# Optimization experiments

Measured on AMD Instinct MI355X. Metric: run time of the kernel, lower is better.

The kernel has to match this reference:

```python
import jax, jax.numpy as jnp
import numpy as np
from jax import lax
from functools import partial

NPOINT = 2048
RADIUS = 1.0
NSAMPLE = 32


def _fps(xyz, npoint):
    # Farthest point sampling, sequential as in the classic CUDA kernel.
    # xyz: (N, 3) -> (npoint,) int32 indices; starts at index 0.
    N = xyz.shape[0]
    init_d = jnp.full((N,), jnp.inf, dtype=xyz.dtype)

    def step(carry, _):
        dists, last = carry
        delta = xyz - xyz[last]                      # (N, 3)
        nd = jnp.sum(delta * delta, axis=-1)         # (N,)
        dists = jnp.minimum(dists, nd)
        nxt = jnp.argmax(dists).astype(jnp.int32)
        return (dists, nxt), last

    (_, _), idxs = lax.scan(step, (init_d, jnp.int32(0)), None, length=npoint)
    return idxs


def _ball_query(radius, nsample, xyz, new_xyz):
    # xyz: (N, 3), new_xyz: (S, 3) -> (S, nsample) int32.
    # Take the first nsample points (in original order) within radius of each
    # centroid; pad with the first found index (centroid itself always hits).
    N = xyz.shape[0]
    d2 = (jnp.sum(new_xyz * new_xyz, -1, keepdims=True)
          + jnp.sum(xyz * xyz, -1)[None, :]
          - 2.0 * new_xyz @ xyz.T)                   # (S, N)
    mask = d2 < radius * radius
    key = jnp.where(mask, jnp.arange(N, dtype=jnp.int32), jnp.int32(N))  # (S, N)
    neg_topk, _ = lax.top_k(-key, nsample)           # nsample smallest keys
    idx = -neg_topk                                  # (S, nsample), ascending
    first = idx[:, :1]
    return jnp.where(idx == N, first, idx)


def setup_inputs() -> dict:
    key = jax.random.key(0)
    inputs = jax.random.normal(key, (4, 8192, 16), dtype=jnp.float32)
    return {"inputs": inputs}


def reference(inputs):
    xyz = inputs[..., :3]                            # (B, N, 3)
    points = inputs[..., 3:]                         # (B, N, C)

    fps_idx = jax.vmap(lambda p: _fps(p, NPOINT))(xyz)          # (B, S)
    new_xyz = jnp.take_along_axis(xyz, fps_idx[..., None], axis=1)  # (B, S, 3)

    idx = jax.vmap(partial(_ball_query, RADIUS, NSAMPLE))(xyz, new_xyz)  # (B, S, K)

    gather = jax.vmap(lambda p, i: p[i])             # (N, C), (S, K) -> (S, K, C)
    grouped_xyz = gather(xyz, idx) - new_xyz[:, :, None, :]      # (B, S, K, 3)
    grouped_points = gather(points, idx)                         # (B, S, K, C)
    new_points = jnp.concatenate([grouped_xyz, grouped_points], axis=-1)
    return new_xyz, new_points, idx, grouped_xyz
```

## Files before the change

### kernel.cpp

```cpp
#include <hip/hip_runtime.h>

#pragma clang fp contract(off)

#define NPOINT 2048
#define NSAMPLE 32
#define NPTS 8192
#define NB 4
#define CH 16
#define FPS_THREADS 512
#define PTS_PER_THREAD (NPTS / FPS_THREADS)
#define PAIRS (PTS_PER_THREAD / 2)

typedef unsigned long long u64;
typedef float v2f __attribute__((ext_vector_type(2)));

#define OFF_NEWXYZ 0
#define OFF_NEWPTS (NB * NPOINT * 3)
#define OFF_IDX (OFF_NEWPTS + NB * NPOINT * NSAMPLE * CH)
#define OFF_GXYZ (OFF_IDX + NB * NPOINT * NSAMPLE)

template <int CTRL>
__device__ __forceinline__ float dpp_fmax(float v) {
  int o = __builtin_amdgcn_update_dpp(0, __float_as_int(v), CTRL, 0xf, 0xf, true);
  return fmaxf(v, __int_as_float(o));
}

__global__ __launch_bounds__(FPS_THREADS)
__attribute__((amdgpu_waves_per_eu(2))) void fps_kernel(
    const float* __restrict__ in, float* __restrict__ out) {
  __shared__ float4 lpxyz[NPTS];
  __shared__ float newb[NPOINT * 3];
  __shared__ u64 kslot[3];

  const int b = blockIdx.x;
  const int tid = threadIdx.x;
  const float* base = in + (size_t)b * NPTS * CH;

  v2f pxv[PAIRS], pyv[PAIRS], pzv[PAIRS], dv[PAIRS];
#pragma unroll
  for (int jp = 0; jp < PAIRS; ++jp) {
    int p0 = tid * PTS_PER_THREAD + 2 * jp;
    float4 r0 = *reinterpret_cast<const float4*>(base + (size_t)p0 * CH);
    float4 r1 = *reinterpret_cast<const float4*>(base + (size_t)(p0 + 1) * CH);
    pxv[jp] = (v2f){r0.x, r1.x};
    pyv[jp] = (v2f){r0.y, r1.y};
    pzv[jp] = (v2f){r0.z, r1.z};
    lpxyz[p0] = r0;
    lpxyz[p0 + 1] = r1;
    dv[jp] = (v2f){__builtin_inff(), __builtin_inff()};
  }
  if (tid == 0) {
    kslot[0] = ((u64)0x7f800000u << 32) | 8191u;
    kslot[1] = 0;
    kslot[2] = 0;
  }

  int rd = 0, at = 1, rs = 2;
  for (int it = 0; it < NPOINT; ++it) {
    __syncthreads();
    const u64 k = kslot[rd];
    const int gi = 8191 - (int)(unsigned)k;
    const float4 g = lpxyz[gi];
    const float gx = g.x, gy = g.y, gz = g.z;
    if (tid == 0) {
      kslot[rs] = 0;
      newb[it * 3 + 0] = gx;
      newb[it * 3 + 1] = gy;
      newb[it * 3 + 2] = gz;
    }
    float bestv = -1.0f;
#pragma unroll
    for (int jp = 0; jp < PAIRS; ++jp) {
      v2f dx = pxv[jp] - gx;
      v2f dy = pyv[jp] - gy;
      v2f dz = pzv[jp] - gz;
      v2f nd = (dx * dx + dy * dy) + dz * dz;
      v2f dn = {fminf(dv[jp].x, nd.x), fminf(dv[jp].y, nd.y)};
      dv[jp] = dn;
      bestv = fmaxf(fmaxf(bestv, dn.x), dn.y);
    }
    const float* df = (const float*)dv;
    int bestj = 0;
#pragma unroll
    for (int jj = PTS_PER_THREAD - 1; jj >= 0; --jj)
      if (df[jj] == bestv) bestj = jj;
    const int besti = tid * PTS_PER_THREAD + bestj;
    float wm = bestv;
    wm = dpp_fmax<0x111>(wm);
    wm = dpp_fmax<0x112>(wm);
    wm = dpp_fmax<0x114>(wm);
    wm = dpp_fmax<0x118>(wm);
    wm = dpp_fmax<0x142>(wm);
    wm = dpp_fmax<0x143>(wm);
    const float swm =
        __int_as_float(__builtin_amdgcn_readlane(__float_as_int(wm), 63));
    if (bestv == swm) {
      u64 key = ((u64)__float_as_uint(bestv) << 32) | (8191u - (unsigned)besti);
      atomicMax(&kslot[at], key);
    }
    const int t = rd;
    rd = at;
    at = rs;
    rs = t;
  }
  __syncthreads();
  float* ob = out + OFF_NEWXYZ + (size_t)b * NPOINT * 3;
  for (int i = tid; i < NPOINT * 3; i += FPS_THREADS) ob[i] = newb[i];
}

__device__ __forceinline__ void write_slot(float* __restrict__ out,
                                           const float* __restrict__ base,
                                           int b, int qi, int s, int p,
                                           float4 r0, float qx, float qy,
                                           float qz) {
  float dx = __fsub_rn(r0.x, qx);
  float dy = __fsub_rn(r0.y, qy);
  float dz = __fsub_rn(r0.z, qz);
  size_t qs = (size_t)b * NPOINT + qi;
  out[OFF_IDX + qs * NSAMPLE + s] = (float)p;
  float* g = out + OFF_GXYZ + (qs * NSAMPLE + s) * 3;
  g[0] = dx;
  g[1] = dy;
  g[2] = dz;
  const float* row = base + (size_t)p * CH;
  float4 r1 = *reinterpret_cast<const float4*>(row + 4);
  float4 r2 = *reinterpret_cast<const float4*>(row + 8);
  float4 r3 = *reinterpret_cast<const float4*>(row + 12);
  float* np_ = out + OFF_NEWPTS + (qs * NSAMPLE + s) * CH;
  *reinterpret_cast<float4*>(np_ + 0) = make_float4(dx, dy, dz, r0.w);
  *reinterpret_cast<float4*>(np_ + 4) = r1;
  *reinterpret_cast<float4*>(np_ + 8) = r2;
  *reinterpret_cast<float4*>(np_ + 12) = r3;
}

__global__ __launch_bounds__(256) void ballq_kernel(
    const float* __restrict__ in, float* __restrict__ out) {
  const int lane = threadIdx.x & 63;
  const int qid = blockIdx.x * 4 + (threadIdx.x >> 6);
  const int b = qid >> 11;
  const int qi = qid & 2047;
  const float* base = in + (size_t)b * NPTS * CH;
  const float* q = out + OFF_NEWXYZ + ((size_t)b * NPOINT + qi) * 3;
  float qx = q[0], qy = q[1], qz = q[2];
  float qn = __fadd_rn(__fadd_rn(__fmul_rn(qx, qx), __fmul_rn(qy, qy)),
                       __fmul_rn(qz, qz));

  int cnt = 0;
  int first = 0;
  bool have_first = false;
  for (int chunk = 0; chunk < NPTS / 64 && cnt < NSAMPLE; ++chunk) {
    int p = chunk * 64 + lane;
    float4 r0 = *reinterpret_cast<const float4*>(base + (size_t)p * CH);
    float pn =
        __fadd_rn(__fadd_rn(__fmul_rn(r0.x, r0.x), __fmul_rn(r0.y, r0.y)),
                  __fmul_rn(r0.z, r0.z));
    float dot =
        __fadd_rn(__fadd_rn(__fmul_rn(qx, r0.x), __fmul_rn(qy, r0.y)),
                  __fmul_rn(qz, r0.z));
    float d2 = __fsub_rn(__fadd_rn(qn, pn), __fmul_rn(2.0f, dot));
    bool in_r = d2 < 1.0f;
    unsigned long long mask = __ballot(in_r);
    if (!have_first && mask) {
      first = chunk * 64 + __builtin_ctzll(mask);
      have_first = true;
    }
    int pos = cnt + __popcll(mask & ((1ull << lane) - 1ull));
    if (in_r && pos < NSAMPLE) write_slot(out, base, b, qi, pos, p, r0, qx, qy, qz);
    cnt += __popcll(mask);
  }
  if (cnt < NSAMPLE) {
    int s = cnt + lane;
    if (s < NSAMPLE) {
      float4 r0 = *reinterpret_cast<const float4*>(base + (size_t)first * CH);
      write_slot(out, base, b, qi, s, first, r0, qx, qy, qz);
    }
  }
}

extern "C" void kernel_launch(void* const* d_in, const int* in_sizes, int n_in,
                              void* d_out, int out_size, void* d_ws,
                              size_t ws_size, hipStream_t stream) {
  (void)in_sizes;
  (void)n_in;
  (void)out_size;
  (void)d_ws;
  (void)ws_size;
  const float* in = (const float*)d_in[0];
  float* out = (float*)d_out;
  fps_kernel<<<NB, FPS_THREADS, 0, stream>>>(in, out);
  ballq_kernel<<<(NB * NPOINT) / 4, 256, 0, stream>>>(in, out);
}
```

Baseline: 2.093 ms.

## Halve FPS block threads, fuse argmax tracking, one atomic per wave

Cuts the farthest-point-sampling block from 512 to 256 threads, so each thread holds 32 points in scalar registers instead of packed float2 pairs, and relaxes the occupancy hint to one wave per EU. The running argmax index is now tracked inside the distance loop instead of in a separate rescan. Each wave then picks its lowest winning lane with a ballot and issues one atomicMax from lane 0, instead of every tied lane issuing its own. The aim is fewer waves per barrier and less atomic and scan overhead per iteration, at the cost of twice the serial work per thread and losing the packed float math.

```diff
diff --git a/kernel.cpp b/kernel.cpp
--- a/kernel.cpp
+++ b/kernel.cpp
@@ -7,12 +7,10 @@
 #define NPTS 8192
 #define NB 4
 #define CH 16
-#define FPS_THREADS 512
+#define FPS_THREADS 256
 #define PTS_PER_THREAD (NPTS / FPS_THREADS)
-#define PAIRS (PTS_PER_THREAD / 2)
 
 typedef unsigned long long u64;
-typedef float v2f __attribute__((ext_vector_type(2)));
 
 #define OFF_NEWXYZ 0
 #define OFF_NEWPTS (NB * NPOINT * 3)
@@ -26,7 +24,7 @@
 }
 
 __global__ __launch_bounds__(FPS_THREADS)
-__attribute__((amdgpu_waves_per_eu(2))) void fps_kernel(
+__attribute__((amdgpu_waves_per_eu(1))) void fps_kernel(
     const float* __restrict__ in, float* __restrict__ out) {
   __shared__ float4 lpxyz[NPTS];
   __shared__ float newb[NPOINT * 3];
@@ -34,20 +32,20 @@
 
   const int b = blockIdx.x;
   const int tid = threadIdx.x;
+  const int lane = tid & 63;
   const float* base = in + (size_t)b * NPTS * CH;
 
-  v2f pxv[PAIRS], pyv[PAIRS], pzv[PAIRS], dv[PAIRS];
+  float px[PTS_PER_THREAD], py[PTS_PER_THREAD], pz[PTS_PER_THREAD],
+      d[PTS_PER_THREAD];
 #pragma unroll
-  for (int jp = 0; jp < PAIRS; ++jp) {
-    int p0 = tid * PTS_PER_THREAD + 2 * jp;
-    float4 r0 = *reinterpret_cast<const float4*>(base + (size_t)p0 * CH);
-    float4 r1 = *reinterpret_cast<const float4*>(base + (size_t)(p0 + 1) * CH);
-    pxv[jp] = (v2f){r0.x, r1.x};
-    pyv[jp] = (v2f){r0.y, r1.y};
-    pzv[jp] = (v2f){r0.z, r1.z};
-    lpxyz[p0] = r0;
-    lpxyz[p0 + 1] = r1;
-    dv[jp] = (v2f){__builtin_inff(), __builtin_inff()};
+  for (int j = 0; j < PTS_PER_THREAD; ++j) {
+    int p = tid * PTS_PER_THREAD + j;
+    float4 r = *reinterpret_cast<const float4*>(base + (size_t)p * CH);
+    px[j] = r.x;
+    py[j] = r.y;
+    pz[j] = r.z;
+    lpxyz[p] = r;
+    d[j] = __builtin_inff();
   }
   if (tid == 0) {
     kslot[0] = ((u64)0x7f800000u << 32) | 8191u;
@@ -69,21 +67,18 @@
       newb[it * 3 + 2] = gz;
     }
     float bestv = -1.0f;
-#pragma unroll
-    for (int jp = 0; jp < PAIRS; ++jp) {
-      v2f dx = pxv[jp] - gx;
-      v2f dy = pyv[jp] - gy;
-      v2f dz = pzv[jp] - gz;
-      v2f nd = (dx * dx + dy * dy) + dz * dz;
-      v2f dn = {fminf(dv[jp].x, nd.x), fminf(dv[jp].y, nd.y)};
-      dv[jp] = dn;
-      bestv = fmaxf(fmaxf(bestv, dn.x), dn.y);
-    }
-    const float* df = (const float*)dv;
     int bestj = 0;
 #pragma unroll
-    for (int jj = PTS_PER_THREAD - 1; jj >= 0; --jj)
-      if (df[jj] == bestv) bestj = jj;
+    for (int j = 0; j < PTS_PER_THREAD; ++j) {
+      float dx = px[j] - gx;
+      float dy = py[j] - gy;
+      float dz = pz[j] - gz;
+      float nd = (dx * dx + dy * dy) + dz * dz;
+      float dn = fminf(d[j], nd);
+      d[j] = dn;
+      bestj = (dn > bestv) ? j : bestj;
+      bestv = fmaxf(bestv, dn);
+    }
     const int besti = tid * PTS_PER_THREAD + bestj;
     float wm = bestv;
     wm = dpp_fmax<0x111>(wm);
@@ -94,8 +89,11 @@
     wm = dpp_fmax<0x143>(wm);
     const float swm =
         __int_as_float(__builtin_amdgcn_readlane(__float_as_int(wm), 63));
-    if (bestv == swm) {
-      u64 key = ((u64)__float_as_uint(bestv) << 32) | (8191u - (unsigned)besti);
+    const u64 wbal = __ballot(bestv == swm);
+    const int wl = (int)__builtin_ctzll(wbal);
+    const int widx = __builtin_amdgcn_readlane(besti, wl);
+    if (lane == 0) {
+      u64 key = ((u64)__float_as_uint(swm) << 32) | (8191u - (unsigned)widx);
       atomicMax(&kslot[at], key);
     }
     const int t = rd;
```

Result: faster. 1.917 ms (-8.4%).

## Replace shared atomicMax argmax with per-wave slots and halve FPS block size

Applied to the files above, without the earlier changes.

The FPS block shrinks from 512 to 256 threads, so each thread holds 32 points, and the waves-per-EU hint drops to 1. The shared-memory atomicMax on a triple-buffered key becomes per-wave slots in a double buffer. Each wave's lowest-index winning lane writes its packed key, and every thread reduces the four slots after the barrier. The per-thread index search now runs only in that winning lane, which removes LDS atomics and the work in losing lanes from the serial 2048-iteration loop. The cost is twice the distance work per thread and more register pressure.

```diff
diff --git a/kernel.cpp b/kernel.cpp
--- a/kernel.cpp
+++ b/kernel.cpp
@@ -7,9 +7,10 @@
 #define NPTS 8192
 #define NB 4
 #define CH 16
-#define FPS_THREADS 512
+#define FPS_THREADS 256
 #define PTS_PER_THREAD (NPTS / FPS_THREADS)
 #define PAIRS (PTS_PER_THREAD / 2)
+#define FPS_WAVES (FPS_THREADS / 64)
 
 typedef unsigned long long u64;
 typedef float v2f __attribute__((ext_vector_type(2)));
@@ -26,14 +27,16 @@
 }
 
 __global__ __launch_bounds__(FPS_THREADS)
-__attribute__((amdgpu_waves_per_eu(2))) void fps_kernel(
+__attribute__((amdgpu_waves_per_eu(1))) void fps_kernel(
     const float* __restrict__ in, float* __restrict__ out) {
   __shared__ float4 lpxyz[NPTS];
   __shared__ float newb[NPOINT * 3];
-  __shared__ u64 kslot[3];
+  __shared__ alignas(16) u64 slots[2][FPS_WAVES];
 
   const int b = blockIdx.x;
   const int tid = threadIdx.x;
+  const int lane = tid & 63;
+  const int wv = tid >> 6;
   const float* base = in + (size_t)b * NPTS * CH;
 
   v2f pxv[PAIRS], pyv[PAIRS], pzv[PAIRS], dv[PAIRS];
@@ -49,21 +52,23 @@
     lpxyz[p0 + 1] = r1;
     dv[jp] = (v2f){__builtin_inff(), __builtin_inff()};
   }
-  if (tid == 0) {
-    kslot[0] = ((u64)0x7f800000u << 32) | 8191u;
-    kslot[1] = 0;
-    kslot[2] = 0;
-  }
+  if (tid < FPS_WAVES)
+    slots[0][tid] = (tid == 0) ? (((u64)0x7f800000u << 32) | 8191u) : 0ull;
 
-  int rd = 0, at = 1, rs = 2;
   for (int it = 0; it < NPOINT; ++it) {
     __syncthreads();
-    const u64 k = kslot[rd];
+    const ulonglong2 s01 =
+        *reinterpret_cast<const ulonglong2*>(&slots[it & 1][0]);
+    const ulonglong2 s23 =
+        *reinterpret_cast<const ulonglong2*>(&slots[it & 1][2]);
+    u64 k = s01.x;
+    k = (s01.y > k) ? s01.y : k;
+    k = (s23.x > k) ? s23.x : k;
+    k = (s23.y > k) ? s23.y : k;
     const int gi = 8191 - (int)(unsigned)k;
     const float4 g = lpxyz[gi];
     const float gx = g.x, gy = g.y, gz = g.z;
     if (tid == 0) {
-      kslot[rs] = 0;
       newb[it * 3 + 0] = gx;
       newb[it * 3 + 1] = gy;
       newb[it * 3 + 2] = gz;
@@ -77,14 +82,8 @@
       v2f nd = (dx * dx + dy * dy) + dz * dz;
       v2f dn = {fminf(dv[jp].x, nd.x), fminf(dv[jp].y, nd.y)};
       dv[jp] = dn;
-      bestv = fmaxf(fmaxf(bestv, dn.x), dn.y);
+      bestv = fmaxf(bestv, fmaxf(dn.x, dn.y));
     }
-    const float* df = (const float*)dv;
-    int bestj = 0;
-#pragma unroll
-    for (int jj = PTS_PER_THREAD - 1; jj >= 0; --jj)
-      if (df[jj] == bestv) bestj = jj;
-    const int besti = tid * PTS_PER_THREAD + bestj;
     float wm = bestv;
     wm = dpp_fmax<0x111>(wm);
     wm = dpp_fmax<0x112>(wm);
@@ -94,14 +93,18 @@
     wm = dpp_fmax<0x143>(wm);
     const float swm =
         __int_as_float(__builtin_amdgcn_readlane(__float_as_int(wm), 63));
-    if (bestv == swm) {
-      u64 key = ((u64)__float_as_uint(bestv) << 32) | (8191u - (unsigned)besti);
-      atomicMax(&kslot[at], key);
+    const u64 wbal = __ballot(bestv == swm);
+    const int wl = (int)__builtin_ctzll(wbal);
+    if (lane == wl) {
+      const float* df = (const float*)dv;
+      int bestj = 0;
+#pragma unroll
+      for (int jj = PTS_PER_THREAD - 1; jj >= 0; --jj)
+        if (df[jj] == bestv) bestj = jj;
+      const unsigned besti = (unsigned)(tid * PTS_PER_THREAD + bestj);
+      slots[(it + 1) & 1][wv] =
+          ((u64)__float_as_uint(bestv) << 32) | (8191u - besti);
     }
-    const int t = rd;
-    rd = at;
-    at = rs;
-    rs = t;
   }
   __syncthreads();
   float* ob = out + OFF_NEWXYZ + (size_t)b * NPOINT * 3;
```

After: 2.376 ms. 13.5% more time.
